# Kernel tuning notes

Measured on AMD Instinct MI355X. Metric: run time of the kernel, lower is better.

## Reference

```python
import jax, jax.numpy as jnp
import numpy as np

K = 6  # hardcoded top-k in the original forward


def setup_inputs() -> dict:
    key = jax.random.key(0)
    k1, k2, k3, k4, k5 = jax.random.split(key, 5)
    N, M, C = 512, 2048, 256
    return {
        "micro": jax.random.normal(k1, (N, C), jnp.float32),
        "label": jax.random.uniform(k2, (N,), jnp.float32),
        "micro_all": jax.random.normal(k3, (M, C), jnp.float32),
        "label_all": jax.random.uniform(k4, (M,), jnp.float32),
        # fc = nn.Linear(channels, 1, bias=False) -> weight vector [C]
        "fc_w": jax.random.normal(k5, (C,), jnp.float32) * 0.05,
    }


def reference(micro, label, micro_all, label_all, fc_w):
    N, C = micro.shape
    M = micro_all.shape[0]
    # Pairwise squared differences: dis[n, m, c] = (micro_all[m,c] - micro[n,c])^2
    dis = (micro_all[None, :, :] - micro[:, None, :]) ** 2  # [N, M, C]
    # Linear(C,1,bias=False) along channel dim, minus per-pair channel mean
    anti = jnp.einsum('nmc,c->nm', dis, fc_w) - dis.mean(axis=2)  # [N, M]
    anti = jax.nn.softmax(anti, axis=1)
    # top-k mask (argsort-based selection of k largest == lax.top_k)
    _, idx = jax.lax.top_k(anti, K)  # [N, K]
    mask = jnp.zeros((N, M), anti.dtype).at[jnp.arange(N)[:, None], idx].set(1.0)
    cut = anti * mask
    cut = cut / jnp.sum(cut, axis=1, keepdims=True)  # renormalize kNN weights
    micro_tmp = micro + cut @ micro_all  # [N, C]
    # composition loss
    dis_label = jnp.abs(label_all[None, :] - label[:, None])  # [N, M]
    co_loss = jnp.asarray(1e-4, cut.dtype) + jnp.sum(dis_label * cut) / N
    return micro_tmp, co_loss
```

## Files before the change

kernel.cpp:

```cpp
#include <hip/hip_runtime.h>
#include <hip/hip_bf16.h>
#include <math.h>

#define N_Q   512
#define M_ALL 2048
#define CHN   256
#define TOPK  6
#define NREF  10
#define INV_C (1.0f / 256.0f)

#define WS_AW_F    4096
#define WS_BIAS_F  (WS_AW_F + (M_ALL * CHN) / 2)
#define WS_BMIC_F  (WS_BIAS_F + M_ALL)
#define WS_LOGIT_F (WS_BMIC_F + (N_Q * CHN) / 2)

typedef __bf16 bf16x8 __attribute__((ext_vector_type(8)));
typedef float  f32x4  __attribute__((ext_vector_type(4)));

static __device__ __forceinline__ unsigned short bfbits(float x) {
    __bf16 h = (__bf16)x;
    unsigned short u;
    __builtin_memcpy(&u, &h, 2);
    return u;
}

static __device__ __forceinline__ unsigned key_of(float f, int m) {
    unsigned u = __float_as_uint(f);
    u = (u & 0x80000000u) ? ~u : (u | 0x80000000u);
    return (u & 0xFFFFF800u) | (unsigned)m;
}

__global__ __launch_bounds__(256) void gcn_prep(
    const float* __restrict__ micro_all,
    const float* __restrict__ micro,
    const float* __restrict__ fc_w,
    unsigned short* __restrict__ aw,
    float* __restrict__ bias,
    unsigned short* __restrict__ bmic,
    float* __restrict__ out)
{
    const int t    = threadIdx.x;
    const int wave = t >> 6;
    const int lane = t & 63;

    if (blockIdx.x == 0 && t == 0) out[N_Q * CHN] = 1e-4f;

    if (blockIdx.x < M_ALL / 4) {
        const int row = blockIdx.x * 4 + wave;
        const float4 a = *(const float4*)(micro_all + (size_t)row * CHN + lane * 4);
        float4 w = *(const float4*)(fc_w + lane * 4);
        w.x -= INV_C; w.y -= INV_C; w.z -= INV_C; w.w -= INV_C;

        const float sx = a.x * w.x, sy = a.y * w.y, sz = a.z * w.z, sw = a.w * w.w;
        ushort4 pk;
        pk.x = bfbits(sx); pk.y = bfbits(sy); pk.z = bfbits(sz); pk.w = bfbits(sw);
        *(ushort4*)(aw + (size_t)row * CHN + lane * 4) = pk;

        float p = a.x * sx + a.y * sy + a.z * sz + a.w * sw;
        #pragma unroll
        for (int mask = 32; mask >= 1; mask >>= 1)
            p += __shfl_xor(p, mask, 64);
        if (lane == 0) bias[row] = p;
    } else {
        const int row = (blockIdx.x - M_ALL / 4) * 4 + wave;
        const float4 a = *(const float4*)(micro + (size_t)row * CHN + lane * 4);
        ushort4 pk;
        pk.x = bfbits(a.x); pk.y = bfbits(a.y); pk.z = bfbits(a.z); pk.w = bfbits(a.w);
        *(ushort4*)(bmic + (size_t)row * CHN + lane * 4) = pk;
    }
}

#define BM 64
#define BN 32

__global__ __launch_bounds__(256) void gcn_gemm(
    const unsigned short* __restrict__ aw,
    const float* __restrict__ bias,
    const unsigned short* __restrict__ bmic,
    float* __restrict__ logits)
{
    const int t    = threadIdx.x;
    const int w    = t >> 6;
    const int l15  = t & 15;
    const int quad = (t >> 4) & 3;
    const int m0   = blockIdx.x * BM;
    const int n0   = blockIdx.y * BN;

    const int nt  = w & 1;
    const int mtp = w >> 1;

    const unsigned short* brow  = bmic + (size_t)(n0 + nt * 16 + l15) * CHN;
    const unsigned short* arow0 = aw + (size_t)(m0 + mtp * 32 + l15) * CHN;
    const unsigned short* arow1 = arow0 + 16 * CHN;

    f32x4 acc0 = {0.f, 0.f, 0.f, 0.f};
    f32x4 acc1 = {0.f, 0.f, 0.f, 0.f};
    #pragma unroll
    for (int ks = 0; ks < 8; ++ks) {
        const int k0 = ks * 32 + quad * 8;
        const bf16x8 a  = *(const bf16x8*)(brow + k0);
        const bf16x8 b0 = *(const bf16x8*)(arow0 + k0);
        const bf16x8 b1 = *(const bf16x8*)(arow1 + k0);
        acc0 = __builtin_amdgcn_mfma_f32_16x16x32_bf16(a, b0, acc0, 0, 0, 0);
        acc1 = __builtin_amdgcn_mfma_f32_16x16x32_bf16(a, b1, acc1, 0, 0, 0);
    }

    const float bias0 = bias[m0 + mtp * 32 + l15];
    const float bias1 = bias[m0 + mtp * 32 + 16 + l15];
    #pragma unroll
    for (int reg = 0; reg < 4; ++reg) {
        const int n = n0 + nt * 16 + quad * 4 + reg;
        logits[(size_t)n * M_ALL + m0 + mtp * 32 + l15]      = bias0 - 2.f * acc0[reg];
        logits[(size_t)n * M_ALL + m0 + mtp * 32 + 16 + l15] = bias1 - 2.f * acc1[reg];
    }
}

#define BLOCK 256
#define WAVES (BLOCK / 64)
#define MPT   (M_ALL / BLOCK)
#define WTOP  8
#define NCAND (WAVES * WTOP)

__global__ __launch_bounds__(BLOCK) void gcn_topk(
    const float* __restrict__ logits,
    const float* __restrict__ micro,
    const float* __restrict__ label,
    const float* __restrict__ micro_all,
    const float* __restrict__ label_all,
    const float* __restrict__ fc_w,
    float* __restrict__ out)
{
    __shared__ unsigned s_keys[NCAND];
    __shared__ unsigned s_top[NREF];
    __shared__ float    s_ex[NREF];

    const int n    = blockIdx.x;
    const int t    = threadIdx.x;
    const int wave = t >> 6;
    const int lane = t & 63;

    const float4 b4 = *(const float4*)(micro + (size_t)n * CHN + lane * 4);
    float4 w4 = *(const float4*)(fc_w + lane * 4);
    w4.x -= INV_C; w4.y -= INV_C; w4.z -= INV_C; w4.w -= INV_C;

    unsigned k8[MPT];
    {
        const float4 v0 = *(const float4*)(logits + (size_t)n * M_ALL + t * 8);
        const float4 v1 = *(const float4*)(logits + (size_t)n * M_ALL + t * 8 + 4);
        const int mb = t * 8;
        k8[0] = key_of(v0.x, mb + 0);
        k8[1] = key_of(v0.y, mb + 1);
        k8[2] = key_of(v0.z, mb + 2);
        k8[3] = key_of(v0.w, mb + 3);
        k8[4] = key_of(v1.x, mb + 4);
        k8[5] = key_of(v1.y, mb + 5);
        k8[6] = key_of(v1.z, mb + 6);
        k8[7] = key_of(v1.w, mb + 7);
    }

    #pragma unroll
    for (int k = 0; k < WTOP; ++k) {
        unsigned best = k8[0];
        #pragma unroll
        for (int j = 1; j < MPT; ++j) best = (k8[j] > best) ? k8[j] : best;
        #pragma unroll
        for (int mask = 32; mask > 0; mask >>= 1) {
            const unsigned ov = __shfl_xor(best, mask, 64);
            best = (ov > best) ? ov : best;
        }
        if (lane == 0) s_keys[wave * WTOP + k] = best;
        #pragma unroll
        for (int j = 0; j < MPT; ++j)
            k8[j] = (k8[j] == best) ? 0u : k8[j];
    }
    __syncthreads();

    {
        unsigned v = s_keys[lane & 31];
        #pragma unroll
        for (int k = 2; k <= 32; k <<= 1) {
            #pragma unroll
            for (int j = k >> 1; j >= 1; j >>= 1) {
                const unsigned pv = __shfl_xor(v, j, 64);
                const unsigned mx = (v > pv) ? v : pv;
                const unsigned mn = (v > pv) ? pv : v;
                const bool up    = ((lane & k) == 0);
                const bool lower = ((lane & j) == 0);
                v = (up == lower) ? mx : mn;
            }
        }
        if (wave == 0 && lane < NREF) s_top[lane] = v;
    }
    __syncthreads();

    for (int c = wave; c < NREF; c += WAVES) {
        const int m = (int)(s_top[c] & 0x7FFu);
        const float4 a = *(const float4*)(micro_all + (size_t)m * CHN + lane * 4);
        const float dx = a.x - b4.x;
        const float dy = a.y - b4.y;
        const float dz = a.z - b4.z;
        const float dw = a.w - b4.w;
        float acc = dx * dx * w4.x + dy * dy * w4.y + dz * dz * w4.z + dw * dw * w4.w;
        #pragma unroll
        for (int mask = 32; mask >= 1; mask >>= 1)
            acc += __shfl_xor(acc, mask, 64);
        if (lane == 0) s_ex[c] = acc;
    }
    __syncthreads();

    float top_val[TOPK];
    int   top_idx[TOPK];
    unsigned rtk = 0u;
    #pragma unroll
    for (int k = 0; k < TOPK; ++k) {
        float best = -INFINITY;
        int   bi   = 0;
        #pragma unroll
        for (int c = 0; c < NREF; ++c) {
            const bool avail = ((rtk >> c) & 1u) == 0u;
            const float cv = s_ex[c];
            if (avail && cv > best) { best = cv; bi = c; }
        }
        top_val[k] = best;
        top_idx[k] = (int)(s_top[bi] & 0x7FFu);
        rtk |= 1u << bi;
    }

    const float mx = top_val[0];
    float e[TOPK];
    float esum = 0.0f;
    #pragma unroll
    for (int k = 0; k < TOPK; ++k) { e[k] = __expf(top_val[k] - mx); esum += e[k]; }
    const float inv = 1.0f / esum;

    float outv = micro[(size_t)n * CHN + t];
    #pragma unroll
    for (int k = 0; k < TOPK; ++k)
        outv += (e[k] * inv) * micro_all[(size_t)top_idx[k] * CHN + t];
    out[n * CHN + t] = outv;

    if (t == 0) {
        const float lab = label[n];
        float l = 0.0f;
        #pragma unroll
        for (int k = 0; k < TOPK; ++k)
            l += (e[k] * inv) * fabsf(label_all[top_idx[k]] - lab);
        atomicAdd(out + N_Q * CHN, l * (1.0f / (float)N_Q));
    }
}

extern "C" void kernel_launch(void* const* d_in, const int* in_sizes, int n_in,
                              void* d_out, int out_size, void* d_ws, size_t ws_size,
                              hipStream_t stream) {
    const float* micro     = (const float*)d_in[0];
    const float* label     = (const float*)d_in[1];
    const float* micro_all = (const float*)d_in[2];
    const float* label_all = (const float*)d_in[3];
    const float* fc_w      = (const float*)d_in[4];
    float* out  = (float*)d_out;
    float* ws   = (float*)d_ws;
    unsigned short* aw     = (unsigned short*)(ws + WS_AW_F);
    float*          bias   = ws + WS_BIAS_F;
    unsigned short* bmic   = (unsigned short*)(ws + WS_BMIC_F);
    float*          logits = ws + WS_LOGIT_F;

    gcn_prep<<<M_ALL / 4 + N_Q / 4, 256, 0, stream>>>(
        micro_all, micro, fc_w, aw, bias, bmic, out);
    gcn_gemm<<<dim3(M_ALL / BM, N_Q / BN), 256, 0, stream>>>(
        aw, bias, bmic, logits);
    gcn_topk<<<N_Q, BLOCK, 0, stream>>>(logits, micro, label, micro_all,
                                        label_all, fc_w, out);
}
```

Measured before the change: 88.57 us.

## Fuse prep, GEMM and top-k into one persistent kernel with grid barriers

Merges the three launches (bf16 prep, MFMA logits GEMM, per-row top-k/output) into a single 256-block persistent kernel. The stages are separated by software grid barriers built on atomic counters, which are cleared with a memset before the launch. Each block now handles 8 micro_all rows, 2 micro rows, two GEMM tiles with the B fragment kept in registers, and two query rows of top-k. The aim is to remove kernel launch gaps. In exchange it adds a memset, spin-wait barriers, and fewer blocks per stage, and it depends on all 256 blocks being resident at the same time.

```diff
diff --git a/kernel.cpp b/kernel.cpp
--- a/kernel.cpp
+++ b/kernel.cpp
@@ -8,6 +8,7 @@
 #define TOPK  6
 #define NREF  10
 #define INV_C (1.0f / 256.0f)
+#define NBLK  256
 
 #define WS_AW_F    4096
 #define WS_BIAS_F  (WS_AW_F + (M_ALL * CHN) / 2)
@@ -30,222 +31,238 @@
     return (u & 0xFFFFF800u) | (unsigned)m;
 }
 
-__global__ __launch_bounds__(256) void gcn_prep(
+static __device__ __forceinline__ void grid_sync(unsigned* bar) {
+    __syncthreads();
+    if (threadIdx.x == 0) {
+        __threadfence();
+        const unsigned arrived = atomicAdd(bar, 1u) + 1u;
+        if (arrived < NBLK) {
+            while (__hip_atomic_load(bar, __ATOMIC_RELAXED,
+                                     __HIP_MEMORY_SCOPE_AGENT) < NBLK)
+                __builtin_amdgcn_s_sleep(2);
+        }
+        __threadfence();
+    }
+    __syncthreads();
+}
+
+#define BLOCK 256
+#define WAVES 4
+#define MPT   (M_ALL / BLOCK)
+#define WTOP  8
+#define NCAND (WAVES * WTOP)
+
+__global__ __launch_bounds__(256) void gcn_fused(
     const float* __restrict__ micro_all,
     const float* __restrict__ micro,
     const float* __restrict__ fc_w,
+    const float* __restrict__ label,
+    const float* __restrict__ label_all,
     unsigned short* __restrict__ aw,
     float* __restrict__ bias,
     unsigned short* __restrict__ bmic,
-    float* __restrict__ out)
-{
-    const int t    = threadIdx.x;
-    const int wave = t >> 6;
-    const int lane = t & 63;
-
-    if (blockIdx.x == 0 && t == 0) out[N_Q * CHN] = 1e-4f;
-
-    if (blockIdx.x < M_ALL / 4) {
-        const int row = blockIdx.x * 4 + wave;
-        const float4 a = *(const float4*)(micro_all + (size_t)row * CHN + lane * 4);
-        float4 w = *(const float4*)(fc_w + lane * 4);
-        w.x -= INV_C; w.y -= INV_C; w.z -= INV_C; w.w -= INV_C;
-
-        const float sx = a.x * w.x, sy = a.y * w.y, sz = a.z * w.z, sw = a.w * w.w;
-        ushort4 pk;
-        pk.x = bfbits(sx); pk.y = bfbits(sy); pk.z = bfbits(sz); pk.w = bfbits(sw);
-        *(ushort4*)(aw + (size_t)row * CHN + lane * 4) = pk;
-
-        float p = a.x * sx + a.y * sy + a.z * sz + a.w * sw;
-        #pragma unroll
-        for (int mask = 32; mask >= 1; mask >>= 1)
-            p += __shfl_xor(p, mask, 64);
-        if (lane == 0) bias[row] = p;
-    } else {
-        const int row = (blockIdx.x - M_ALL / 4) * 4 + wave;
-        const float4 a = *(const float4*)(micro + (size_t)row * CHN + lane * 4);
-        ushort4 pk;
-        pk.x = bfbits(a.x); pk.y = bfbits(a.y); pk.z = bfbits(a.z); pk.w = bfbits(a.w);
-        *(ushort4*)(bmic + (size_t)row * CHN + lane * 4) = pk;
-    }
-}
-
-#define BM 64
-#define BN 32
-
-__global__ __launch_bounds__(256) void gcn_gemm(
-    const unsigned short* __restrict__ aw,
-    const float* __restrict__ bias,
-    const unsigned short* __restrict__ bmic,
-    float* __restrict__ logits)
-{
-    const int t    = threadIdx.x;
-    const int w    = t >> 6;
-    const int l15  = t & 15;
-    const int quad = (t >> 4) & 3;
-    const int m0   = blockIdx.x * BM;
-    const int n0   = blockIdx.y * BN;
-
-    const int nt  = w & 1;
-    const int mtp = w >> 1;
-
-    const unsigned short* brow  = bmic + (size_t)(n0 + nt * 16 + l15) * CHN;
-    const unsigned short* arow0 = aw + (size_t)(m0 + mtp * 32 + l15) * CHN;
-    const unsigned short* arow1 = arow0 + 16 * CHN;
-
-    f32x4 acc0 = {0.f, 0.f, 0.f, 0.f};
-    f32x4 acc1 = {0.f, 0.f, 0.f, 0.f};
-    #pragma unroll
-    for (int ks = 0; ks < 8; ++ks) {
-        const int k0 = ks * 32 + quad * 8;
-        const bf16x8 a  = *(const bf16x8*)(brow + k0);
-        const bf16x8 b0 = *(const bf16x8*)(arow0 + k0);
-        const bf16x8 b1 = *(const bf16x8*)(arow1 + k0);
-        acc0 = __builtin_amdgcn_mfma_f32_16x16x32_bf16(a, b0, acc0, 0, 0, 0);
-        acc1 = __builtin_amdgcn_mfma_f32_16x16x32_bf16(a, b1, acc1, 0, 0, 0);
-    }
-
-    const float bias0 = bias[m0 + mtp * 32 + l15];
-    const float bias1 = bias[m0 + mtp * 32 + 16 + l15];
-    #pragma unroll
-    for (int reg = 0; reg < 4; ++reg) {
-        const int n = n0 + nt * 16 + quad * 4 + reg;
-        logits[(size_t)n * M_ALL + m0 + mtp * 32 + l15]      = bias0 - 2.f * acc0[reg];
-        logits[(size_t)n * M_ALL + m0 + mtp * 32 + 16 + l15] = bias1 - 2.f * acc1[reg];
-    }
-}
-
-#define BLOCK 256
-#define WAVES (BLOCK / 64)
-#define MPT   (M_ALL / BLOCK)
-#define WTOP  8
-#define NCAND (WAVES * WTOP)
-
-__global__ __launch_bounds__(BLOCK) void gcn_topk(
-    const float* __restrict__ logits,
-    const float* __restrict__ micro,
-    const float* __restrict__ label,
-    const float* __restrict__ micro_all,
-    const float* __restrict__ label_all,
-    const float* __restrict__ fc_w,
-    float* __restrict__ out)
+    float* __restrict__ logits,
+    float* __restrict__ out,
+    unsigned* __restrict__ bar)
 {
     __shared__ unsigned s_keys[NCAND];
     __shared__ unsigned s_top[NREF];
     __shared__ float    s_ex[NREF];
 
-    const int n    = blockIdx.x;
+    const int b    = blockIdx.x;
     const int t    = threadIdx.x;
-    const int wave = t >> 6;
+    const int w    = t >> 6;
     const int lane = t & 63;
-
-    const float4 b4 = *(const float4*)(micro + (size_t)n * CHN + lane * 4);
+    const int l15  = lane & 15;
+    const int quad = lane >> 4;
+
+    {
+        float4 wv = *(const float4*)(fc_w + lane * 4);
+        wv.x -= INV_C; wv.y -= INV_C; wv.z -= INV_C; wv.w -= INV_C;
+
+        #pragma unroll
+        for (int r2 = 0; r2 < 2; ++r2) {
+            const int row = b * 8 + w * 2 + r2;
+            const float4 a = *(const float4*)(micro_all + (size_t)row * CHN + lane * 4);
+            const float sx = a.x * wv.x, sy = a.y * wv.y, sz = a.z * wv.z, sw = a.w * wv.w;
+            ushort4 pk;
+            pk.x = bfbits(sx); pk.y = bfbits(sy); pk.z = bfbits(sz); pk.w = bfbits(sw);
+            *(ushort4*)(aw + (size_t)row * CHN + lane * 4) = pk;
+
+            float p = a.x * sx + a.y * sy + a.z * sz + a.w * sw;
+            #pragma unroll
+            for (int mask = 32; mask >= 1; mask >>= 1)
+                p += __shfl_xor(p, mask, 64);
+            if (lane == 0) bias[row] = p;
+        }
+
+        if (w < 2) {
+            const int row = b * 2 + w;
+            const float4 a = *(const float4*)(micro + (size_t)row * CHN + lane * 4);
+            ushort4 pk;
+            pk.x = bfbits(a.x); pk.y = bfbits(a.y); pk.z = bfbits(a.z); pk.w = bfbits(a.w);
+            *(ushort4*)(bmic + (size_t)row * CHN + lane * 4) = pk;
+        }
+
+        if (b == 0 && t == 0) out[N_Q * CHN] = 1e-4f;
+    }
+    grid_sync(bar + 0);
+
+    {
+        const int n0  = ((2 * b) >> 5) * 32;
+        const int nt  = w & 1;
+        const int mtp = w >> 1;
+
+        const unsigned short* brow = bmic + (size_t)(n0 + nt * 16 + l15) * CHN;
+        bf16x8 bq[8];
+        #pragma unroll
+        for (int ks = 0; ks < 8; ++ks)
+            bq[ks] = *(const bf16x8*)(brow + ks * 32 + quad * 8);
+
+        #pragma unroll
+        for (int ti = 0; ti < 2; ++ti) {
+            const int tau = 2 * b + ti;
+            const int m0  = (tau & 31) * 64;
+
+            const unsigned short* arow0 = aw + (size_t)(m0 + mtp * 32 + l15) * CHN;
+            const unsigned short* arow1 = arow0 + 16 * CHN;
+
+            f32x4 acc0 = {0.f, 0.f, 0.f, 0.f};
+            f32x4 acc1 = {0.f, 0.f, 0.f, 0.f};
+            #pragma unroll
+            for (int ks = 0; ks < 8; ++ks) {
+                const int k0 = ks * 32 + quad * 8;
+                const bf16x8 b0 = *(const bf16x8*)(arow0 + k0);
+                const bf16x8 b1 = *(const bf16x8*)(arow1 + k0);
+                acc0 = __builtin_amdgcn_mfma_f32_16x16x32_bf16(bq[ks], b0, acc0, 0, 0, 0);
+                acc1 = __builtin_amdgcn_mfma_f32_16x16x32_bf16(bq[ks], b1, acc1, 0, 0, 0);
+            }
+
+            const float bias0 = bias[m0 + mtp * 32 + l15];
+            const float bias1 = bias[m0 + mtp * 32 + 16 + l15];
+            #pragma unroll
+            for (int reg = 0; reg < 4; ++reg) {
+                const int n = n0 + nt * 16 + quad * 4 + reg;
+                logits[(size_t)n * M_ALL + m0 + mtp * 32 + l15]      = bias0 - 2.f * acc0[reg];
+                logits[(size_t)n * M_ALL + m0 + mtp * 32 + 16 + l15] = bias1 - 2.f * acc1[reg];
+            }
+        }
+    }
+    grid_sync(bar + 1);
+
     float4 w4 = *(const float4*)(fc_w + lane * 4);
     w4.x -= INV_C; w4.y -= INV_C; w4.z -= INV_C; w4.w -= INV_C;
 
-    unsigned k8[MPT];
-    {
-        const float4 v0 = *(const float4*)(logits + (size_t)n * M_ALL + t * 8);
-        const float4 v1 = *(const float4*)(logits + (size_t)n * M_ALL + t * 8 + 4);
-        const int mb = t * 8;
-        k8[0] = key_of(v0.x, mb + 0);
-        k8[1] = key_of(v0.y, mb + 1);
-        k8[2] = key_of(v0.z, mb + 2);
-        k8[3] = key_of(v0.w, mb + 3);
-        k8[4] = key_of(v1.x, mb + 4);
-        k8[5] = key_of(v1.y, mb + 5);
-        k8[6] = key_of(v1.z, mb + 6);
-        k8[7] = key_of(v1.w, mb + 7);
-    }
-
-    #pragma unroll
-    for (int k = 0; k < WTOP; ++k) {
-        unsigned best = k8[0];
-        #pragma unroll
-        for (int j = 1; j < MPT; ++j) best = (k8[j] > best) ? k8[j] : best;
-        #pragma unroll
-        for (int mask = 32; mask > 0; mask >>= 1) {
-            const unsigned ov = __shfl_xor(best, mask, 64);
-            best = (ov > best) ? ov : best;
-        }
-        if (lane == 0) s_keys[wave * WTOP + k] = best;
-        #pragma unroll
-        for (int j = 0; j < MPT; ++j)
-            k8[j] = (k8[j] == best) ? 0u : k8[j];
-    }
-    __syncthreads();
-
-    {
-        unsigned v = s_keys[lane & 31];
-        #pragma unroll
-        for (int k = 2; k <= 32; k <<= 1) {
-            #pragma unroll
-            for (int j = k >> 1; j >= 1; j >>= 1) {
-                const unsigned pv = __shfl_xor(v, j, 64);
-                const unsigned mx = (v > pv) ? v : pv;
-                const unsigned mn = (v > pv) ? pv : v;
-                const bool up    = ((lane & k) == 0);
-                const bool lower = ((lane & j) == 0);
-                v = (up == lower) ? mx : mn;
-            }
-        }
-        if (wave == 0 && lane < NREF) s_top[lane] = v;
-    }
-    __syncthreads();
-
-    for (int c = wave; c < NREF; c += WAVES) {
-        const int m = (int)(s_top[c] & 0x7FFu);
-        const float4 a = *(const float4*)(micro_all + (size_t)m * CHN + lane * 4);
-        const float dx = a.x - b4.x;
-        const float dy = a.y - b4.y;
-        const float dz = a.z - b4.z;
-        const float dw = a.w - b4.w;
-        float acc = dx * dx * w4.x + dy * dy * w4.y + dz * dz * w4.z + dw * dw * w4.w;
-        #pragma unroll
-        for (int mask = 32; mask >= 1; mask >>= 1)
-            acc += __shfl_xor(acc, mask, 64);
-        if (lane == 0) s_ex[c] = acc;
-    }
-    __syncthreads();
-
-    float top_val[TOPK];
-    int   top_idx[TOPK];
-    unsigned rtk = 0u;
-    #pragma unroll
-    for (int k = 0; k < TOPK; ++k) {
-        float best = -INFINITY;
-        int   bi   = 0;
-        #pragma unroll
-        for (int c = 0; c < NREF; ++c) {
-            const bool avail = ((rtk >> c) & 1u) == 0u;
-            const float cv = s_ex[c];
-            if (avail && cv > best) { best = cv; bi = c; }
-        }
-        top_val[k] = best;
-        top_idx[k] = (int)(s_top[bi] & 0x7FFu);
-        rtk |= 1u << bi;
-    }
-
-    const float mx = top_val[0];
-    float e[TOPK];
-    float esum = 0.0f;
-    #pragma unroll
-    for (int k = 0; k < TOPK; ++k) { e[k] = __expf(top_val[k] - mx); esum += e[k]; }
-    const float inv = 1.0f / esum;
-
-    float outv = micro[(size_t)n * CHN + t];
-    #pragma unroll
-    for (int k = 0; k < TOPK; ++k)
-        outv += (e[k] * inv) * micro_all[(size_t)top_idx[k] * CHN + t];
-    out[n * CHN + t] = outv;
-
-    if (t == 0) {
-        const float lab = label[n];
-        float l = 0.0f;
+    for (int it = 0; it < 2; ++it) {
+        const int n = 2 * b + it;
+        __syncthreads();
+
+        const float4 b4 = *(const float4*)(micro + (size_t)n * CHN + lane * 4);
+
+        unsigned k8[MPT];
+        {
+            const float4 v0 = *(const float4*)(logits + (size_t)n * M_ALL + t * 8);
+            const float4 v1 = *(const float4*)(logits + (size_t)n * M_ALL + t * 8 + 4);
+            const int mb = t * 8;
+            k8[0] = key_of(v0.x, mb + 0);
+            k8[1] = key_of(v0.y, mb + 1);
+            k8[2] = key_of(v0.z, mb + 2);
+            k8[3] = key_of(v0.w, mb + 3);
+            k8[4] = key_of(v1.x, mb + 4);
+            k8[5] = key_of(v1.y, mb + 5);
+            k8[6] = key_of(v1.z, mb + 6);
+            k8[7] = key_of(v1.w, mb + 7);
+        }
+
+        #pragma unroll
+        for (int k = 0; k < WTOP; ++k) {
+            unsigned best = k8[0];
+            #pragma unroll
+            for (int j = 1; j < MPT; ++j) best = (k8[j] > best) ? k8[j] : best;
+            #pragma unroll
+            for (int mask = 32; mask > 0; mask >>= 1) {
+                const unsigned ov = __shfl_xor(best, mask, 64);
+                best = (ov > best) ? ov : best;
+            }
+            if (lane == 0) s_keys[w * WTOP + k] = best;
+            #pragma unroll
+            for (int j = 0; j < MPT; ++j)
+                k8[j] = (k8[j] == best) ? 0u : k8[j];
+        }
+        __syncthreads();
+
+        {
+            unsigned v = s_keys[lane & 31];
+            #pragma unroll
+            for (int k = 2; k <= 32; k <<= 1) {
+                #pragma unroll
+                for (int j = k >> 1; j >= 1; j >>= 1) {
+                    const unsigned pv = __shfl_xor(v, j, 64);
+                    const unsigned mx = (v > pv) ? v : pv;
+                    const unsigned mn = (v > pv) ? pv : v;
+                    const bool up    = ((lane & k) == 0);
+                    const bool lower = ((lane & j) == 0);
+                    v = (up == lower) ? mx : mn;
+                }
+            }
+            if (w == 0 && lane < NREF) s_top[lane] = v;
+        }
+        __syncthreads();
+
+        for (int c = w; c < NREF; c += WAVES) {
+            const int m = (int)(s_top[c] & 0x7FFu);
+            const float4 a = *(const float4*)(micro_all + (size_t)m * CHN + lane * 4);
+            const float dx = a.x - b4.x;
+            const float dy = a.y - b4.y;
+            const float dz = a.z - b4.z;
+            const float dw = a.w - b4.w;
+            float acc = dx * dx * w4.x + dy * dy * w4.y + dz * dz * w4.z + dw * dw * w4.w;
+            #pragma unroll
+            for (int mask = 32; mask >= 1; mask >>= 1)
+                acc += __shfl_xor(acc, mask, 64);
+            if (lane == 0) s_ex[c] = acc;
+        }
+        __syncthreads();
+
+        float top_val[TOPK];
+        int   top_idx[TOPK];
+        unsigned rtk = 0u;
+        #pragma unroll
+        for (int k = 0; k < TOPK; ++k) {
+            float best = -INFINITY;
+            int   bi   = 0;
+            #pragma unroll
+            for (int c = 0; c < NREF; ++c) {
+                const bool avail = ((rtk >> c) & 1u) == 0u;
+                const float cv = s_ex[c];
+                if (avail && cv > best) { best = cv; bi = c; }
+            }
+            top_val[k] = best;
+            top_idx[k] = (int)(s_top[bi] & 0x7FFu);
+            rtk |= 1u << bi;
+        }
+
+        const float mx = top_val[0];
+        float e[TOPK];
+        float esum = 0.0f;
+        #pragma unroll
+        for (int k = 0; k < TOPK; ++k) { e[k] = __expf(top_val[k] - mx); esum += e[k]; }
+        const float inv = 1.0f / esum;
+
+        float outv = micro[(size_t)n * CHN + t];
         #pragma unroll
         for (int k = 0; k < TOPK; ++k)
-            l += (e[k] * inv) * fabsf(label_all[top_idx[k]] - lab);
-        atomicAdd(out + N_Q * CHN, l * (1.0f / (float)N_Q));
+            outv += (e[k] * inv) * micro_all[(size_t)top_idx[k] * CHN + t];
+        out[(size_t)n * CHN + t] = outv;
+
+        if (t == 0) {
+            const float lab = label[n];
+            float l = 0.0f;
+            #pragma unroll
+            for (int k = 0; k < TOPK; ++k)
+                l += (e[k] * inv) * fabsf(label_all[top_idx[k]] - lab);
+            atomicAdd(out + N_Q * CHN, l * (1.0f / (float)N_Q));
+        }
     }
 }
 
@@ -259,15 +276,14 @@
     const float* fc_w      = (const float*)d_in[4];
     float* out  = (float*)d_out;
     float* ws   = (float*)d_ws;
+
+    unsigned*       bar    = (unsigned*)ws;
     unsigned short* aw     = (unsigned short*)(ws + WS_AW_F);
     float*          bias   = ws + WS_BIAS_F;
     unsigned short* bmic   = (unsigned short*)(ws + WS_BMIC_F);
     float*          logits = ws + WS_LOGIT_F;
 
-    gcn_prep<<<M_ALL / 4 + N_Q / 4, 256, 0, stream>>>(
-        micro_all, micro, fc_w, aw, bias, bmic, out);
-    gcn_gemm<<<dim3(M_ALL / BM, N_Q / BN), 256, 0, stream>>>(
-        aw, bias, bmic, logits);
-    gcn_topk<<<N_Q, BLOCK, 0, stream>>>(logits, micro, label, micro_all,
-                                        label_all, fc_w, out);
-}
+    hipMemsetAsync(bar, 0, 2 * sizeof(unsigned), stream);
+    gcn_fused<<<NBLK, BLOCK, 0, stream>>>(micro_all, micro, fc_w, label, label_all,
+                                          aw, bias, bmic, logits, out, bar);
+}
```

Result: slower. 124.5 us (+40.5%).

## Fuse bf16 prep into GEMM kernel, computing scaled rows and bias on the fly

Applied to the files above, without the earlier changes.

Removes the separate prep kernel that wrote bf16-packed scaled micro_all, per-row bias and bf16 micro to workspace. The GEMM now reads fp32 inputs directly, applies the fc_w-minus-mean scaling, converts to bf16 in registers and computes the per-row bias with a partial dot product plus lane shuffles. This drops one launch and the workspace round trip. In exchange, each GEMM block rereads fp32 data (twice the bytes) and repeats the scaling and bias work across the 16 N-tiles.

```diff
diff --git a/kernel.cpp b/kernel.cpp
--- a/kernel.cpp
+++ b/kernel.cpp
@@ -9,20 +9,10 @@
 #define NREF  10
 #define INV_C (1.0f / 256.0f)
 
-#define WS_AW_F    4096
-#define WS_BIAS_F  (WS_AW_F + (M_ALL * CHN) / 2)
-#define WS_BMIC_F  (WS_BIAS_F + M_ALL)
-#define WS_LOGIT_F (WS_BMIC_F + (N_Q * CHN) / 2)
+#define WS_LOGIT_F 4096
 
 typedef __bf16 bf16x8 __attribute__((ext_vector_type(8)));
 typedef float  f32x4  __attribute__((ext_vector_type(4)));
-
-static __device__ __forceinline__ unsigned short bfbits(float x) {
-    __bf16 h = (__bf16)x;
-    unsigned short u;
-    __builtin_memcpy(&u, &h, 2);
-    return u;
-}
 
 static __device__ __forceinline__ unsigned key_of(float f, int m) {
     unsigned u = __float_as_uint(f);
@@ -30,54 +20,22 @@
     return (u & 0xFFFFF800u) | (unsigned)m;
 }
 
-__global__ __launch_bounds__(256) void gcn_prep(
+static __device__ __forceinline__ bf16x8 cvt8(float4 lo, float4 hi) {
+    bf16x8 r;
+    r[0] = (__bf16)lo.x; r[1] = (__bf16)lo.y; r[2] = (__bf16)lo.z; r[3] = (__bf16)lo.w;
+    r[4] = (__bf16)hi.x; r[5] = (__bf16)hi.y; r[6] = (__bf16)hi.z; r[7] = (__bf16)hi.w;
+    return r;
+}
+
+#define BM 64
+#define BN 32
+
+__global__ __launch_bounds__(256) void gcn_gemm(
     const float* __restrict__ micro_all,
     const float* __restrict__ micro,
     const float* __restrict__ fc_w,
-    unsigned short* __restrict__ aw,
-    float* __restrict__ bias,
-    unsigned short* __restrict__ bmic,
+    float* __restrict__ logits,
     float* __restrict__ out)
-{
-    const int t    = threadIdx.x;
-    const int wave = t >> 6;
-    const int lane = t & 63;
-
-    if (blockIdx.x == 0 && t == 0) out[N_Q * CHN] = 1e-4f;
-
-    if (blockIdx.x < M_ALL / 4) {
-        const int row = blockIdx.x * 4 + wave;
-        const float4 a = *(const float4*)(micro_all + (size_t)row * CHN + lane * 4);
-        float4 w = *(const float4*)(fc_w + lane * 4);
-        w.x -= INV_C; w.y -= INV_C; w.z -= INV_C; w.w -= INV_C;
-
-        const float sx = a.x * w.x, sy = a.y * w.y, sz = a.z * w.z, sw = a.w * w.w;
-        ushort4 pk;
-        pk.x = bfbits(sx); pk.y = bfbits(sy); pk.z = bfbits(sz); pk.w = bfbits(sw);
-        *(ushort4*)(aw + (size_t)row * CHN + lane * 4) = pk;
-
-        float p = a.x * sx + a.y * sy + a.z * sz + a.w * sw;
-        #pragma unroll
-        for (int mask = 32; mask >= 1; mask >>= 1)
-            p += __shfl_xor(p, mask, 64);
-        if (lane == 0) bias[row] = p;
-    } else {
-        const int row = (blockIdx.x - M_ALL / 4) * 4 + wave;
-        const float4 a = *(const float4*)(micro + (size_t)row * CHN + lane * 4);
-        ushort4 pk;
-        pk.x = bfbits(a.x); pk.y = bfbits(a.y); pk.z = bfbits(a.z); pk.w = bfbits(a.w);
-        *(ushort4*)(bmic + (size_t)row * CHN + lane * 4) = pk;
-    }
-}
-
-#define BM 64
-#define BN 32
-
-__global__ __launch_bounds__(256) void gcn_gemm(
-    const unsigned short* __restrict__ aw,
-    const float* __restrict__ bias,
-    const unsigned short* __restrict__ bmic,
-    float* __restrict__ logits)
 {
     const int t    = threadIdx.x;
     const int w    = t >> 6;
@@ -86,32 +44,63 @@
     const int m0   = blockIdx.x * BM;
     const int n0   = blockIdx.y * BN;
 
+    if (blockIdx.x == 0 && blockIdx.y == 0 && t == 0)
+        out[N_Q * CHN] = 1e-4f;
+
     const int nt  = w & 1;
     const int mtp = w >> 1;
 
-    const unsigned short* brow  = bmic + (size_t)(n0 + nt * 16 + l15) * CHN;
-    const unsigned short* arow0 = aw + (size_t)(m0 + mtp * 32 + l15) * CHN;
-    const unsigned short* arow1 = arow0 + 16 * CHN;
+    const float* brow  = micro     + (size_t)(n0 + nt * 16 + l15) * CHN;
+    const float* arow0 = micro_all + (size_t)(m0 + mtp * 32 + l15) * CHN;
+    const float* arow1 = arow0 + 16 * CHN;
 
     f32x4 acc0 = {0.f, 0.f, 0.f, 0.f};
     f32x4 acc1 = {0.f, 0.f, 0.f, 0.f};
+    float p0 = 0.0f, p1 = 0.0f;
+
     #pragma unroll
     for (int ks = 0; ks < 8; ++ks) {
         const int k0 = ks * 32 + quad * 8;
-        const bf16x8 a  = *(const bf16x8*)(brow + k0);
-        const bf16x8 b0 = *(const bf16x8*)(arow0 + k0);
-        const bf16x8 b1 = *(const bf16x8*)(arow1 + k0);
-        acc0 = __builtin_amdgcn_mfma_f32_16x16x32_bf16(a, b0, acc0, 0, 0, 0);
-        acc1 = __builtin_amdgcn_mfma_f32_16x16x32_bf16(a, b1, acc1, 0, 0, 0);
-    }
-
-    const float bias0 = bias[m0 + mtp * 32 + l15];
-    const float bias1 = bias[m0 + mtp * 32 + 16 + l15];
+
+        float4 w0 = *(const float4*)(fc_w + k0);
+        float4 w1 = *(const float4*)(fc_w + k0 + 4);
+        w0.x -= INV_C; w0.y -= INV_C; w0.z -= INV_C; w0.w -= INV_C;
+        w1.x -= INV_C; w1.y -= INV_C; w1.z -= INV_C; w1.w -= INV_C;
+
+        const float4 b0 = *(const float4*)(brow + k0);
+        const float4 b1 = *(const float4*)(brow + k0 + 4);
+        const bf16x8 bfr = cvt8(b0, b1);
+
+        {
+            const float4 a0 = *(const float4*)(arow0 + k0);
+            const float4 a1 = *(const float4*)(arow0 + k0 + 4);
+            float4 s0, s1;
+            s0.x = a0.x * w0.x; s0.y = a0.y * w0.y; s0.z = a0.z * w0.z; s0.w = a0.w * w0.w;
+            s1.x = a1.x * w1.x; s1.y = a1.y * w1.y; s1.z = a1.z * w1.z; s1.w = a1.w * w1.w;
+            p0 += a0.x * s0.x + a0.y * s0.y + a0.z * s0.z + a0.w * s0.w
+                + a1.x * s1.x + a1.y * s1.y + a1.z * s1.z + a1.w * s1.w;
+            acc0 = __builtin_amdgcn_mfma_f32_16x16x32_bf16(bfr, cvt8(s0, s1), acc0, 0, 0, 0);
+        }
+        {
+            const float4 a0 = *(const float4*)(arow1 + k0);
+            const float4 a1 = *(const float4*)(arow1 + k0 + 4);
+            float4 s0, s1;
+            s0.x = a0.x * w0.x; s0.y = a0.y * w0.y; s0.z = a0.z * w0.z; s0.w = a0.w * w0.w;
+            s1.x = a1.x * w1.x; s1.y = a1.y * w1.y; s1.z = a1.z * w1.z; s1.w = a1.w * w1.w;
+            p1 += a0.x * s0.x + a0.y * s0.y + a0.z * s0.z + a0.w * s0.w
+                + a1.x * s1.x + a1.y * s1.y + a1.z * s1.z + a1.w * s1.w;
+            acc1 = __builtin_amdgcn_mfma_f32_16x16x32_bf16(bfr, cvt8(s0, s1), acc1, 0, 0, 0);
+        }
+    }
+
+    p0 += __shfl_xor(p0, 16, 64); p0 += __shfl_xor(p0, 32, 64);
+    p1 += __shfl_xor(p1, 16, 64); p1 += __shfl_xor(p1, 32, 64);
+
     #pragma unroll
     for (int reg = 0; reg < 4; ++reg) {
         const int n = n0 + nt * 16 + quad * 4 + reg;
-        logits[(size_t)n * M_ALL + m0 + mtp * 32 + l15]      = bias0 - 2.f * acc0[reg];
-        logits[(size_t)n * M_ALL + m0 + mtp * 32 + 16 + l15] = bias1 - 2.f * acc1[reg];
+        logits[(size_t)n * M_ALL + m0 + mtp * 32 + l15]      = p0 - 2.f * acc0[reg];
+        logits[(size_t)n * M_ALL + m0 + mtp * 32 + 16 + l15] = p1 - 2.f * acc1[reg];
     }
 }
 
@@ -257,17 +246,12 @@
     const float* micro_all = (const float*)d_in[2];
     const float* label_all = (const float*)d_in[3];
     const float* fc_w      = (const float*)d_in[4];
-    float* out  = (float*)d_out;
-    float* ws   = (float*)d_ws;
-    unsigned short* aw     = (unsigned short*)(ws + WS_AW_F);
-    float*          bias   = ws + WS_BIAS_F;
-    unsigned short* bmic   = (unsigned short*)(ws + WS_BMIC_F);
-    float*          logits = ws + WS_LOGIT_F;
-
-    gcn_prep<<<M_ALL / 4 + N_Q / 4, 256, 0, stream>>>(
-        micro_all, micro, fc_w, aw, bias, bmic, out);
+    float* out    = (float*)d_out;
+    float* ws     = (float*)d_ws;
+    float* logits = ws + WS_LOGIT_F;
+
     gcn_gemm<<<dim3(M_ALL / BM, N_Q / BN), 256, 0, stream>>>(
-        aw, bias, bmic, logits);
+        micro_all, micro, fc_w, logits, out);
     gcn_topk<<<N_Q, BLOCK, 0, stream>>>(logits, micro, label, micro_all,
                                         label_all, fc_w, out);
 }
```

New measurement: 91.23 us. 1.03x slower.
